# Kernel tuning notes

Hardware: AMD Instinct MI355X
Metric: run time of the kernel (lower is better)

## Reference

```python
import jax, jax.numpy as jnp
import numpy as np

B, N, P, D, H = 16, 256, 8, 512, 8
E = P * D  # 4096, flattened patch embedding width


def _sincos_pos_embed(q_len, d_model):
    # PatchTST-style 'sincos' positional encoding (learn_pe=False buffer)
    pe = np.zeros((q_len, d_model), dtype=np.float64)
    position = np.arange(q_len, dtype=np.float64)[:, None]
    div_term = np.exp(np.arange(0, d_model, 2, dtype=np.float64) * -(np.log(10000.0) / d_model))
    pe[:, 0::2] = np.sin(position * div_term)
    pe[:, 1::2] = np.cos(position * div_term)
    pe = pe - pe.mean()
    pe = pe / (pe.std() * 10)
    return jnp.asarray(pe, dtype=jnp.float32)


def setup_inputs() -> dict:
    key = jax.random.key(0)
    ks = jax.random.split(key, 10)
    s = 0.02
    return {
        "x": jax.random.normal(ks[0], (B, N, P, D), dtype=jnp.float32),
        "pos_embed": _sincos_pos_embed(N, E),
        "W_embed": jax.random.normal(ks[1], (E, E), dtype=jnp.float32) * s,
        "b_embed": jnp.zeros((E,), dtype=jnp.float32),
        "Wq": jax.random.normal(ks[2], (E, E), dtype=jnp.float32) * s,
        "bq": jnp.zeros((E,), dtype=jnp.float32),
        "Wk": jax.random.normal(ks[3], (E, E), dtype=jnp.float32) * s,
        "bk": jnp.zeros((E,), dtype=jnp.float32),
        "Wv": jax.random.normal(ks[4], (E, E), dtype=jnp.float32) * s,
        "bv": jnp.zeros((E,), dtype=jnp.float32),
        "Wo": jax.random.normal(ks[5], (E, E), dtype=jnp.float32) * s,
        "bo": jnp.zeros((E,), dtype=jnp.float32),
    }


def reference(x, pos_embed, W_embed, b_embed, Wq, bq, Wk, bk, Wv, bv, Wo, bo):
    b, n, p, d = x.shape
    h = H
    dh = E // h  # per-head dim = patch_size * d_keys
    xe = x.reshape(b, n, p * d)                       # B N (P D)
    xe = xe @ W_embed.T + b_embed                     # embed_linear
    xe = xe + pos_embed                               # pos embed (dropout=0, eval)
    q = (xe @ Wq.T + bq).reshape(b, n, h, dh)
    k = (xe @ Wk.T + bk).reshape(b, n, h, dh)
    v = (xe @ Wv.T + bv).reshape(b, n, h, dh)
    scale = 1.0 / np.sqrt(d // h)                     # NOTE: uses d_model//H, not E//H (faithful)
    attn_scores = jnp.einsum('bnhd,bmhd->bhnm', q, k) * scale
    attn_weights = jax.nn.softmax(attn_scores, axis=-1)
    out = jnp.einsum('bhnm,bmhd->bnhd', attn_weights, v).reshape(b, n, h * dh)
    out = out @ Wo.T + bo
    out = out.reshape(b, n, p, d)
    return out, attn_weights
```

## Files before the change

### kernel.cpp

```cpp
#include <hip/hip_runtime.h>
#include <hip/hip_bf16.h>


typedef unsigned short u16;
typedef _Float16 f16;
typedef __attribute__((ext_vector_type(8))) _Float16 v8h;
typedef __attribute__((ext_vector_type(8))) short vu16x8;
typedef __attribute__((ext_vector_type(4))) float vf32x4;

#define MFMA_F16(a, b, c) __builtin_amdgcn_mfma_f32_16x16x32_f16(a, b, c, 0, 0, 0)

__device__ __forceinline__ void gld16(const void* g, void* l) {
    __builtin_amdgcn_global_load_lds((const __attribute__((address_space(1))) void*)g,
                                     (__attribute__((address_space(3))) void*)l,
                                     16, 0, 0);
}

__global__ __launch_bounds__(256) void tof16(const float* __restrict__ s,
                                             f16* __restrict__ d) {
    const size_t i = ((size_t)blockIdx.x * 256 + threadIdx.x) * 4;
    const float4 v = *(const float4*)(s + i);
    d[i + 0] = (f16)v.x; d[i + 1] = (f16)v.y;
    d[i + 2] = (f16)v.z; d[i + 3] = (f16)v.w;
}

template <int MODE>
__global__ __launch_bounds__(512, 4)
void gemmd_nt(const f16* __restrict__ A, const f16* __restrict__ Bw,
              const float* __restrict__ bias, const float* __restrict__ pos,
              f16* __restrict__ Ch, float* __restrict__ Cf) {
    __shared__ __align__(16) u16 sA[2][8192];
    __shared__ __align__(16) u16 sB[2][4096];
    const int t = threadIdx.x;
    const int lane = t & 63, w = t >> 6;
    const int wm = w >> 1, wn = w & 1;
    const int l15 = lane & 15, lg = lane >> 4;
    const int wg = ((blockIdx.x & 7) << 6) + (blockIdx.x >> 3);
    const int m0 = (wg >> 5) << 8, n0 = (wg & 31) << 7;

    int aRow[2], aCol[2];
#pragma unroll
    for (int i = 0; i < 2; ++i) {
        const int c = t + (i << 9);
        const int lr = c >> 3;
        const int v = (c & 7) ^ (lr & 7);
        aRow[i] = ((v >> 2) << 7) + lr;
        aCol[i] = (v & 3) << 3;
    }
    int bRow, bCol;
    {
        const int c = t;
        const int lr = c >> 3;
        const int v = (c & 7) ^ (lr & 7);
        bRow = ((v >> 2) << 6) + lr;
        bCol = (v & 3) << 3;
    }
    const int rA = (wm << 6) + l15;
    const int rB = (wn << 6) + l15;
    const int cA = ((((wm >> 1) << 2) + lg) ^ (rA & 7)) << 3;
    const int cB = (((wn << 2) + lg) ^ (rB & 7)) << 3;
    const int lrA = ((wm & 1) << 6) + l15;
    const int lrB = l15;

    vf32x4 acc[4][4] = {};

#define STG(buf, k0) do {                                                      \
    _Pragma("unroll")                                                          \
    for (int i = 0; i < 2; ++i)                                                \
        gld16(A + (((size_t)(m0 + aRow[i])) << 12) + (k0) + aCol[i],           \
              &sA[buf][(t + (i << 9)) * 8]);                                   \
    gld16(Bw + (((size_t)(n0 + bRow)) << 12) + (k0) + bCol,                    \
          &sB[buf][t * 8]);                                                    \
} while (0)

    STG(0, 0);

    for (int kt = 0; kt < 128; ++kt) {
        const int cb = kt & 1;
        if (kt < 127) {
            STG(cb ^ 1, (kt + 1) << 5);
            asm volatile("s_waitcnt vmcnt(3)" ::: "memory");
        } else {
            asm volatile("s_waitcnt vmcnt(0)" ::: "memory");
        }
        __builtin_amdgcn_s_barrier();
        asm volatile("" ::: "memory");
        v8h av[4], bv[4];
#pragma unroll
        for (int m = 0; m < 4; ++m)
            av[m] = *(const v8h*)(&sA[cb][((lrA + m * 16) << 6) + cA]);
#pragma unroll
        for (int n = 0; n < 4; ++n)
            bv[n] = *(const v8h*)(&sB[cb][((lrB + n * 16) << 6) + cB]);
        asm volatile("s_waitcnt lgkmcnt(0)" ::: "memory");
        __builtin_amdgcn_sched_barrier(0);
        __builtin_amdgcn_s_setprio(1);
#pragma unroll
        for (int m = 0; m < 4; ++m)
#pragma unroll
            for (int n = 0; n < 4; ++n)
                acc[m][n] = MFMA_F16(av[m], bv[n], acc[m][n]);
        __builtin_amdgcn_s_setprio(0);
        __builtin_amdgcn_s_barrier();
        asm volatile("" ::: "memory");
    }
#undef STG

#pragma unroll
    for (int n = 0; n < 4; ++n) {
        const int col = n0 + (wn << 6) + (n << 4) + l15;
        const float bvv = bias[col];
#pragma unroll
        for (int m = 0; m < 4; ++m) {
#pragma unroll
            for (int r = 0; r < 4; ++r) {
                const int row = m0 + (wm << 6) + (m << 4) + (lg << 2) + r;
                float v = acc[m][n][r] + bvv;
                if (MODE == 0) v += pos[((size_t)(row & 255) << 12) + col];
                if (MODE == 2)
                    Cf[((size_t)row << 12) + col] = v;
                else
                    Ch[((size_t)row << 12) + col] = (f16)v;
            }
        }
    }
}

__global__ __launch_bounds__(256)
void attn_scores(const f16* __restrict__ q, const f16* __restrict__ k,
                 float* __restrict__ Pf, f16* __restrict__ Pb) {
    const int blk = ((blockIdx.x & 7) << 6) + (blockIdx.x >> 3);
    const int bh = blk >> 2, it = blk & 3;
    const int b = bh >> 3, h = bh & 7;
    const size_t qoff = ((size_t)(b * 256 + it * 64) << 12) + (h << 9);
    const size_t koff = ((size_t)(b * 256) << 12) + (h << 9);
    __shared__ __align__(16) u16 Qs[64 * 64];
    __shared__ __align__(16) u16 Ks[256 * 64];
    __shared__ float red[4][64];

    const int t = threadIdx.x;
    const int lane = t & 63, w = t >> 6;
    const int l15 = lane & 15, lg = lane >> 4;

    vf32x4 acc[4][4] = {};

    for (int k0 = 0; k0 < 512; k0 += 64) {
#pragma unroll
        for (int i = 0; i < 2; ++i) {
            const int c = t + (i << 8);
            const int row = c >> 3, c8 = (c & 7) << 3;
            gld16(q + qoff + ((size_t)row << 12) + k0 + c8, Qs + c * 8);
        }
#pragma unroll
        for (int i = 0; i < 8; ++i) {
            const int c = t + (i << 8);
            const int row = c >> 3, c8 = (c & 7) << 3;
            gld16(k + koff + ((size_t)row << 12) + k0 + c8, Ks + c * 8);
        }
        __syncthreads();
#pragma unroll
        for (int kk = 0; kk < 2; ++kk) {
            v8h af[4], bf[4];
#pragma unroll
            for (int m = 0; m < 4; ++m)
                af[m] = *(const v8h*)(Qs + (m * 16 + l15) * 64 + kk * 32 + lg * 8);
#pragma unroll
            for (int n = 0; n < 4; ++n)
                bf[n] = *(const v8h*)(Ks + (w * 64 + n * 16 + l15) * 64 + kk * 32 + lg * 8);
#pragma unroll
            for (int m = 0; m < 4; ++m)
#pragma unroll
                for (int n = 0; n < 4; ++n)
                    acc[m][n] = MFMA_F16(af[m], bf[n], acc[m][n]);
        }
        __syncthreads();
    }

#pragma unroll
    for (int m = 0; m < 4; ++m)
#pragma unroll
        for (int n = 0; n < 4; ++n) acc[m][n] *= 0.125f;

    float gm[4][4];
#pragma unroll
    for (int m = 0; m < 4; ++m)
#pragma unroll
        for (int r = 0; r < 4; ++r) {
            float v = fmaxf(fmaxf(acc[m][0][r], acc[m][1][r]),
                            fmaxf(acc[m][2][r], acc[m][3][r]));
#pragma unroll
            for (int off = 1; off < 16; off <<= 1) v = fmaxf(v, __shfl_xor(v, off));
            gm[m][r] = v;
        }
    if (l15 == 0) {
#pragma unroll
        for (int m = 0; m < 4; ++m)
#pragma unroll
            for (int r = 0; r < 4; ++r) red[w][m * 16 + lg * 4 + r] = gm[m][r];
    }
    __syncthreads();
#pragma unroll
    for (int m = 0; m < 4; ++m)
#pragma unroll
        for (int r = 0; r < 4; ++r) {
            const int row = m * 16 + lg * 4 + r;
            gm[m][r] = fmaxf(fmaxf(red[0][row], red[1][row]),
                             fmaxf(red[2][row], red[3][row]));
        }
    __syncthreads();

    float gs[4][4];
#pragma unroll
    for (int m = 0; m < 4; ++m)
#pragma unroll
        for (int r = 0; r < 4; ++r) {
            float s = 0.f;
#pragma unroll
            for (int n = 0; n < 4; ++n) {
                const float e = __expf(acc[m][n][r] - gm[m][r]);
                acc[m][n][r] = e;
                s += e;
            }
#pragma unroll
            for (int off = 1; off < 16; off <<= 1) s += __shfl_xor(s, off);
            gs[m][r] = s;
        }
    if (l15 == 0) {
#pragma unroll
        for (int m = 0; m < 4; ++m)
#pragma unroll
            for (int r = 0; r < 4; ++r) red[w][m * 16 + lg * 4 + r] = gs[m][r];
    }
    __syncthreads();

    const size_t pbase = ((size_t)bh * 256 + it * 64) * 256;
#pragma unroll
    for (int m = 0; m < 4; ++m)
#pragma unroll
        for (int r = 0; r < 4; ++r) {
            const int row = m * 16 + lg * 4 + r;
            const float inv = 1.0f / (red[0][row] + red[1][row] +
                                      red[2][row] + red[3][row]);
#pragma unroll
            for (int n = 0; n < 4; ++n) {
                const int col = w * 64 + n * 16 + l15;
                const float p = acc[m][n][r] * inv;
                Pf[pbase + (size_t)row * 256 + col] = p;
                Pb[pbase + (size_t)row * 256 + col] = (f16)p;
            }
        }
}

__global__ __launch_bounds__(256)
void attn_pv(const f16* __restrict__ P, const f16* __restrict__ V,
             f16* __restrict__ O) {
    __shared__ __align__(16) u16 Ps[128 * 64];
    __shared__ __align__(16) u16 Vt[128 * 72];
    const int t = threadIdx.x;
    const int lane = t & 63, w = t >> 6;
    const int wr = (w >> 1) << 6, wc = (w & 1) << 6;
    const int l15 = lane & 15, lg = lane >> 4;
    const int blk = ((blockIdx.x & 7) << 7) + (blockIdx.x >> 3);
    const int bh = blk >> 3, mt = (blk >> 2) & 1, nt = blk & 3;
    const int b = bh >> 3, h = bh & 7;
    const f16* Pbp = P + ((size_t)bh << 16) + ((size_t)mt << 15);
    const u16* Vb = (const u16*)V + ((size_t)(b * 256) << 12) + (h << 9) + (nt << 7);

    vf32x4 acc[4][4] = {};

    for (int k0 = 0; k0 < 256; k0 += 64) {
#pragma unroll
        for (int i = 0; i < 4; ++i) {
            const int c = t + (i << 8);
            const int row = c >> 3, c8 = (c & 7) << 3;
            gld16(Pbp + (size_t)row * 256 + k0 + c8, Ps + c * 8);
        }
#pragma unroll
        for (int pp = 0; pp < 4; ++pp) {
            const int kr = pp * 16 + (t >> 4);
            const int c8 = (t & 15) << 3;
            vu16x8 vv = *(const vu16x8*)(Vb + ((size_t)(k0 + kr) << 12) + c8);
#pragma unroll
            for (int c = 0; c < 8; ++c) Vt[(c8 + c) * 72 + kr] = (u16)vv[c];
        }
        __syncthreads();
#pragma unroll
        for (int kk = 0; kk < 2; ++kk) {
            v8h af[4], bf[4];
#pragma unroll
            for (int m = 0; m < 4; ++m)
                af[m] = *(const v8h*)(Ps + (wr + m * 16 + l15) * 64 + kk * 32 + lg * 8);
#pragma unroll
            for (int n = 0; n < 4; ++n)
                bf[n] = *(const v8h*)(Vt + (wc + n * 16 + l15) * 72 + kk * 32 + lg * 8);
#pragma unroll
            for (int m = 0; m < 4; ++m)
#pragma unroll
                for (int n = 0; n < 4; ++n)
                    acc[m][n] = MFMA_F16(af[m], bf[n], acc[m][n]);
        }
        __syncthreads();
    }

#pragma unroll
    for (int m = 0; m < 4; ++m)
#pragma unroll
        for (int n = 0; n < 4; ++n) {
            const int col = (h << 9) + (nt << 7) + wc + n * 16 + l15;
#pragma unroll
            for (int r = 0; r < 4; ++r) {
                const int row = b * 256 + mt * 128 + wr + m * 16 + lg * 4 + r;
                O[((size_t)row << 12) + col] = (f16)acc[m][n][r];
            }
        }
}

extern "C" void kernel_launch(void* const* d_in, const int* in_sizes, int n_in,
                              void* d_out, int out_size, void* d_ws, size_t ws_size,
                              hipStream_t stream) {
    const float* x   = (const float*)d_in[0];
    const float* pos = (const float*)d_in[1];
    const float* wE  = (const float*)d_in[2];
    const float* bE  = (const float*)d_in[3];
    const float* wQ  = (const float*)d_in[4];
    const float* bq  = (const float*)d_in[5];
    const float* wK  = (const float*)d_in[6];
    const float* bk  = (const float*)d_in[7];
    const float* wV  = (const float*)d_in[8];
    const float* bv  = (const float*)d_in[9];
    const float* wO  = (const float*)d_in[10];
    const float* bo  = (const float*)d_in[11];

    float* out  = (float*)d_out;
    float* Pout = out + (size_t)16777216;

    char* W = (char*)d_ws;
    const size_t MB = 1024 * 1024;
    f16* xf    = (f16*)(W + 0 * MB);
    f16* wslab = (f16*)(W + 32 * MB);
    f16* xe    = (f16*)(W + 64 * MB);
    f16* qs    = (f16*)(W + 96 * MB);
    f16* ks    = (f16*)(W + 128 * MB);
    f16* vs    = (f16*)(W + 160 * MB);
    f16* Pb    = (f16*)(W + 192 * MB);
    f16* ao    = xf;

    const int CVG = 16384;

    tof16<<<CVG, 256, 0, stream>>>(x, xf);
    tof16<<<CVG, 256, 0, stream>>>(wE, wslab);
    gemmd_nt<0><<<512, 512, 0, stream>>>(xf, wslab, bE, pos, xe, nullptr);

    tof16<<<CVG, 256, 0, stream>>>(wQ, wslab);
    gemmd_nt<1><<<512, 512, 0, stream>>>(xe, wslab, bq, nullptr, qs, nullptr);

    tof16<<<CVG, 256, 0, stream>>>(wK, wslab);
    gemmd_nt<1><<<512, 512, 0, stream>>>(xe, wslab, bk, nullptr, ks, nullptr);

    tof16<<<CVG, 256, 0, stream>>>(wV, wslab);
    gemmd_nt<1><<<512, 512, 0, stream>>>(xe, wslab, bv, nullptr, vs, nullptr);

    attn_scores<<<512, 256, 0, stream>>>(qs, ks, Pout, Pb);
    attn_pv<<<1024, 256, 0, stream>>>(Pb, vs, ao);

    tof16<<<CVG, 256, 0, stream>>>(wO, wslab);
    gemmd_nt<2><<<512, 512, 0, stream>>>(ao, wslab, bo, nullptr, nullptr, out);
}
```

Baseline: 914.9 us.

## Replace double-buffered K=32 GEMM with single-buffered K=64 tiles

```diff
diff --git a/kernel.cpp b/kernel.cpp
--- a/kernel.cpp
+++ b/kernel.cpp
@@ -26,11 +26,11 @@
 
 template <int MODE>
 __global__ __launch_bounds__(512, 4)
-void gemmd_nt(const f16* __restrict__ A, const f16* __restrict__ Bw,
+void gemm4_nt(const f16* __restrict__ A, const f16* __restrict__ Bw,
               const float* __restrict__ bias, const float* __restrict__ pos,
               f16* __restrict__ Ch, float* __restrict__ Cf) {
-    __shared__ __align__(16) u16 sA[2][8192];
-    __shared__ __align__(16) u16 sB[2][4096];
+    __shared__ __align__(16) u16 sA[16384];
+    __shared__ __align__(16) u16 sB[8192];
     const int t = threadIdx.x;
     const int lane = t & 63, w = t >> 6;
     const int wm = w >> 1, wn = w & 1;
@@ -38,73 +38,66 @@
     const int wg = ((blockIdx.x & 7) << 6) + (blockIdx.x >> 3);
     const int m0 = (wg >> 5) << 8, n0 = (wg & 31) << 7;
 
-    int aRow[2], aCol[2];
+    int aRow[4], aCol[4], bRow[2], bCol[2];
+#pragma unroll
+    for (int i = 0; i < 4; ++i) {
+        const int c = t + (i << 9);
+        aRow[i] = c >> 3;
+        aCol[i] = (((c & 7) ^ (aRow[i] & 7)) << 3);
+    }
 #pragma unroll
     for (int i = 0; i < 2; ++i) {
         const int c = t + (i << 9);
-        const int lr = c >> 3;
-        const int v = (c & 7) ^ (lr & 7);
-        aRow[i] = ((v >> 2) << 7) + lr;
-        aCol[i] = (v & 3) << 3;
-    }
-    int bRow, bCol;
-    {
-        const int c = t;
-        const int lr = c >> 3;
-        const int v = (c & 7) ^ (lr & 7);
-        bRow = ((v >> 2) << 6) + lr;
-        bCol = (v & 3) << 3;
+        bRow[i] = c >> 3;
+        bCol[i] = (((c & 7) ^ (bRow[i] & 7)) << 3);
     }
     const int rA = (wm << 6) + l15;
     const int rB = (wn << 6) + l15;
-    const int cA = ((((wm >> 1) << 2) + lg) ^ (rA & 7)) << 3;
-    const int cB = (((wn << 2) + lg) ^ (rB & 7)) << 3;
-    const int lrA = ((wm & 1) << 6) + l15;
-    const int lrB = l15;
+    const int xA = rA & 7, xB = rB & 7;
 
     vf32x4 acc[4][4] = {};
 
-#define STG(buf, k0) do {                                                      \
-    _Pragma("unroll")                                                          \
-    for (int i = 0; i < 2; ++i)                                                \
-        gld16(A + (((size_t)(m0 + aRow[i])) << 12) + (k0) + aCol[i],           \
-              &sA[buf][(t + (i << 9)) * 8]);                                   \
-    gld16(Bw + (((size_t)(n0 + bRow)) << 12) + (k0) + bCol,                    \
-          &sB[buf][t * 8]);                                                    \
-} while (0)
-
-    STG(0, 0);
-
-    for (int kt = 0; kt < 128; ++kt) {
-        const int cb = kt & 1;
-        if (kt < 127) {
-            STG(cb ^ 1, (kt + 1) << 5);
-            asm volatile("s_waitcnt vmcnt(3)" ::: "memory");
-        } else {
-            asm volatile("s_waitcnt vmcnt(0)" ::: "memory");
-        }
+    for (int kt = 0; kt < 64; ++kt) {
+        const int k0 = kt << 6;
+#pragma unroll
+        for (int i = 0; i < 4; ++i) {
+            const int c = t + (i << 9);
+            gld16(A + (((size_t)(m0 + aRow[i])) << 12) + k0 + aCol[i],
+                  &sA[c * 8]);
+        }
+#pragma unroll
+        for (int i = 0; i < 2; ++i) {
+            const int c = t + (i << 9);
+            gld16(Bw + (((size_t)(n0 + bRow[i])) << 12) + k0 + bCol[i],
+                  &sB[c * 8]);
+        }
+        asm volatile("s_waitcnt vmcnt(0)" ::: "memory");
         __builtin_amdgcn_s_barrier();
         asm volatile("" ::: "memory");
-        v8h av[4], bv[4];
-#pragma unroll
-        for (int m = 0; m < 4; ++m)
-            av[m] = *(const v8h*)(&sA[cb][((lrA + m * 16) << 6) + cA]);
-#pragma unroll
-        for (int n = 0; n < 4; ++n)
-            bv[n] = *(const v8h*)(&sB[cb][((lrB + n * 16) << 6) + cB]);
-        asm volatile("s_waitcnt lgkmcnt(0)" ::: "memory");
-        __builtin_amdgcn_sched_barrier(0);
-        __builtin_amdgcn_s_setprio(1);
-#pragma unroll
-        for (int m = 0; m < 4; ++m)
+#pragma unroll
+        for (int kk = 0; kk < 2; ++kk) {
+            const int ccA = (((kk << 2) + lg) ^ xA) << 3;
+            const int ccB = (((kk << 2) + lg) ^ xB) << 3;
+            v8h av[4], bv[4];
+#pragma unroll
+            for (int m = 0; m < 4; ++m)
+                av[m] = *(const v8h*)(&sA[(rA << 6) + (m << 10) + ccA]);
 #pragma unroll
             for (int n = 0; n < 4; ++n)
-                acc[m][n] = MFMA_F16(av[m], bv[n], acc[m][n]);
-        __builtin_amdgcn_s_setprio(0);
+                bv[n] = *(const v8h*)(&sB[(rB << 6) + (n << 10) + ccB]);
+            asm volatile("s_waitcnt lgkmcnt(0)" ::: "memory");
+            __builtin_amdgcn_sched_barrier(0);
+            __builtin_amdgcn_s_setprio(1);
+#pragma unroll
+            for (int m = 0; m < 4; ++m)
+#pragma unroll
+                for (int n = 0; n < 4; ++n)
+                    acc[m][n] = MFMA_F16(av[m], bv[n], acc[m][n]);
+            __builtin_amdgcn_s_setprio(0);
+        }
         __builtin_amdgcn_s_barrier();
         asm volatile("" ::: "memory");
     }
-#undef STG
 
 #pragma unroll
     for (int n = 0; n < 4; ++n) {
@@ -349,20 +342,20 @@
 
     tof16<<<CVG, 256, 0, stream>>>(x, xf);
     tof16<<<CVG, 256, 0, stream>>>(wE, wslab);
-    gemmd_nt<0><<<512, 512, 0, stream>>>(xf, wslab, bE, pos, xe, nullptr);
+    gemm4_nt<0><<<512, 512, 0, stream>>>(xf, wslab, bE, pos, xe, nullptr);
 
     tof16<<<CVG, 256, 0, stream>>>(wQ, wslab);
-    gemmd_nt<1><<<512, 512, 0, stream>>>(xe, wslab, bq, nullptr, qs, nullptr);
+    gemm4_nt<1><<<512, 512, 0, stream>>>(xe, wslab, bq, nullptr, qs, nullptr);
 
     tof16<<<CVG, 256, 0, stream>>>(wK, wslab);
-    gemmd_nt<1><<<512, 512, 0, stream>>>(xe, wslab, bk, nullptr, ks, nullptr);
+    gemm4_nt<1><<<512, 512, 0, stream>>>(xe, wslab, bk, nullptr, ks, nullptr);
 
     tof16<<<CVG, 256, 0, stream>>>(wV, wslab);
-    gemmd_nt<1><<<512, 512, 0, stream>>>(xe, wslab, bv, nullptr, vs, nullptr);
+    gemm4_nt<1><<<512, 512, 0, stream>>>(xe, wslab, bv, nullptr, vs, nullptr);
 
     attn_scores<<<512, 256, 0, stream>>>(qs, ks, Pout, Pb);
     attn_pv<<<1024, 256, 0, stream>>>(Pb, vs, ao);
 
     tof16<<<CVG, 256, 0, stream>>>(wO, wslab);
-    gemmd_nt<2><<<512, 512, 0, stream>>>(ao, wslab, bo, nullptr, nullptr, out);
-}
+    gemm4_nt<2><<<512, 512, 0, stream>>>(ao, wslab, bo, nullptr, nullptr, out);
+}
```

New measurement: 819.7 us. 10.4% less time.
